# Kernel optimization log

Measured on AMD Instinct MI355X. Metric: run time of the kernel, lower is better.

Reference implementation:

```python
import jax, jax.numpy as jnp
import numpy as np


def conv2d(x, w, b):
    # x: [B, Cin, H, W], w: [Cout, Cin, 3, 3] -> SAME 3x3 conv, stride 1
    y = jax.lax.conv_general_dilated(x, w, (1, 1), 'SAME',
                                     dimension_numbers=('NCHW', 'OIHW', 'NCHW'))
    return y + b[None, :, None, None]


def trilinear_interpolation(data, offsets, sample_nums):
    """data: [B, D(frames), C, H, W]; offsets: [B, sample_nums*3, H, W]
    Returns samples [B, sample_nums, C, H, W] via trilinear interp over (d,h,w)."""
    B, D, C, H, W = data.shape
    S = sample_nums
    off = offsets.reshape(B, S, 3, H, W)
    # base 3x3x3 grid centered at middle frame / current pixel
    g = jnp.arange(S)
    kd = (g // 9 - 1).astype(jnp.float32)        # [S]
    kh = ((g // 3) % 3 - 1).astype(jnp.float32)
    kw = (g % 3 - 1).astype(jnp.float32)
    center = (D - 1) / 2.0
    hh = jnp.arange(H, dtype=jnp.float32)
    ww = jnp.arange(W, dtype=jnp.float32)
    pd = center + kd[None, :, None, None] + off[:, :, 0]                 # [B,S,H,W]
    ph = hh[None, None, :, None] + kh[None, :, None, None] + off[:, :, 1]
    pw = ww[None, None, None, :] + kw[None, :, None, None] + off[:, :, 2]
    pd = jnp.clip(pd, 0.0, D - 1.0)
    ph = jnp.clip(ph, 0.0, H - 1.0)
    pw = jnp.clip(pw, 0.0, W - 1.0)
    d0 = jnp.floor(pd); h0 = jnp.floor(ph); w0 = jnp.floor(pw)
    fd = pd - d0; fh = ph - h0; fw = pw - w0
    d0i = d0.astype(jnp.int32); h0i = h0.astype(jnp.int32); w0i = w0.astype(jnp.int32)
    d1i = jnp.minimum(d0i + 1, D - 1)
    h1i = jnp.minimum(h0i + 1, H - 1)
    w1i = jnp.minimum(w0i + 1, W - 1)
    # flatten (d,h,w) for gather, keep channels contiguous
    data_flat = data.transpose(0, 2, 1, 3, 4).reshape(B, C, D * H * W)

    def gather(di, hi, wi):
        idx = ((di * H + hi) * W + wi).reshape(B, 1, S * H * W)
        g_ = jnp.take_along_axis(data_flat, idx, axis=2)   # [B,C,S*H*W]
        return g_.reshape(B, C, S, H, W).transpose(0, 2, 1, 3, 4)  # [B,S,C,H,W]

    out = jnp.zeros((B, S, C, H, W), dtype=data.dtype)
    for di, wd in ((d0i, 1.0 - fd), (d1i, fd)):
        for hi, wh in ((h0i, 1.0 - fh), (h1i, fh)):
            for wi, wwgt in ((w0i, 1.0 - fw), (w1i, fw)):
                wgt = (wd * wh * wwgt)[:, :, None]  # [B,S,1,H,W]
                out = out + wgt * gather(di, hi, wi)
    return out


SAMPLE_NUMS = 27
GROUPS = 3


def setup_inputs() -> dict:
    key = jax.random.key(0)
    ks = jax.random.split(key, 14)
    B, BURST, C, H, W = 4, 5, 3, 256, 256
    in_len = BURST * C          # 15
    ch_w = in_len + 128 + SAMPLE_NUMS * C  # 224
    s = 0.05
    p = lambda k, sh: jax.random.normal(k, sh, dtype=jnp.float32) * s
    return {
        'data': jax.random.normal(ks[0], (B, BURST, C, H, W), dtype=jnp.float32),
        'enc_w1': p(ks[1], (64, in_len, 3, 3)), 'enc_b1': jnp.zeros((64,), jnp.float32),
        'enc_w2': p(ks[2], (128, 64, 3, 3)),    'enc_b2': jnp.zeros((128,), jnp.float32),
        'off_w':  p(ks[3], (SAMPLE_NUMS * 3, 128, 3, 3)), 'off_b': jnp.zeros((SAMPLE_NUMS * 3,), jnp.float32),
        'wc_w1':  p(ks[4], (64, ch_w, 3, 3)),   'wc_b1': jnp.zeros((64,), jnp.float32),
        'wc_w2':  p(ks[5], (64, 64, 3, 3)),     'wc_b2': jnp.zeros((64,), jnp.float32),
        'wc_w3':  p(ks[6], (SAMPLE_NUMS, 64, 3, 3)), 'wc_b3': jnp.zeros((SAMPLE_NUMS,), jnp.float32),
    }


def reference(data, enc_w1, enc_b1, enc_w2, enc_b2, off_w, off_b,
              wc_w1, wc_b1, wc_w2, wc_b2, wc_w3, wc_b3):
    B, D, C, H, W = data.shape
    net_feed = data.reshape(B, D * C, H, W)
    # encoder_decoder proxy: feature [B,128,H,W] + offsets [B,81,H,W]
    f1 = jax.nn.relu(conv2d(net_feed, enc_w1, enc_b1))
    feature = jax.nn.relu(conv2d(f1, enc_w2, enc_b2))
    offsets = conv2d(feature, off_w, off_b)
    samples = trilinear_interpolation(data, offsets, SAMPLE_NUMS)  # [B,S,C,H,W]
    weight_feed = jnp.concatenate([net_feed, feature,
                                   samples.reshape(B, SAMPLE_NUMS * C, H, W)], axis=1)
    h1 = jax.nn.relu(conv2d(weight_feed, wc_w1, wc_b1))
    h2 = jax.nn.relu(conv2d(h1, wc_w2, wc_b2))
    weights = conv2d(h2, wc_w3, wc_b3)  # [B,S,H,W]
    cpg = SAMPLE_NUMS // GROUPS
    s_g = samples.reshape(B, GROUPS, cpg, C, H, W)
    w_g = weights.reshape(B, GROUPS, cpg, H, W)
    # per-group weighted kernel-prediction sum (convolution_3D), scaled by g
    res_i = GROUPS * jnp.einsum('bgkchw,bgkhw->bgchw', s_g, w_g)
    out = jnp.sum(res_i, axis=1) / GROUPS
    return res_i, out, samples
```

## Files before the change

### kernel.cpp

```cpp
#include <hip/hip_runtime.h>


typedef __attribute__((ext_vector_type(8))) short short8;
typedef __attribute__((ext_vector_type(4))) float f32x4;

__device__ __forceinline__ unsigned short f2bf(float f) {
    unsigned int b = __float_as_uint(f);
    b = (b + 0x7fffu + ((b >> 16) & 1u)) >> 16;
    return (unsigned short)b;
}
__device__ __forceinline__ float bf2f(unsigned int u) {
    return __uint_as_float(u << 16);
}
__device__ __forceinline__ unsigned int pack2(float a, float b) {
    return (unsigned int)f2bf(a) | ((unsigned int)f2bf(b) << 16);
}

__global__ __launch_bounds__(256) void pack_w(
    const float* __restrict__ w, unsigned short* __restrict__ wp,
    int Cin_real, int Cout_real, int Cout_pad, int nch, int remap, int total)
{
    int idx = blockIdx.x * 256 + threadIdx.x;
    if (idx >= total) return;
    int kin = idx & 31;
    int t = idx >> 5;
    int co = t % Cout_pad; t /= Cout_pad;
    int chunk = t % nch;
    int tap = t / nch;
    int ci = chunk * 32 + kin;
    int cs = -1;
    if (remap) {
        if (ci < 15) cs = ci;
        else if (ci >= 16 && ci <= 224) cs = ci - 1;
    } else {
        if (ci < Cin_real) cs = ci;
    }
    float val = 0.f;
    if (co < Cout_real && cs >= 0)
        val = w[(co * Cin_real + cs) * 9 + tap];
    wp[idx] = f2bf(val);
}

__global__ __launch_bounds__(256) void convert_data(
    const float* __restrict__ data, unsigned short* __restrict__ concat)
{
    int i = blockIdx.x * 256 + threadIdx.x;
    int b = i >> 16, p = i & 65535;
    int base = i * 232;
#pragma unroll
    for (int c = 0; c < 15; ++c)
        concat[base + c] = f2bf(data[(b * 15 + c) * 65536 + p]);
    concat[base + 15] = 0;
}

__global__ __launch_bounds__(256) void conv_mfma(
    const unsigned short* __restrict__ src, int srcCs, int srcOff,
    const unsigned short* __restrict__ wp, const float* __restrict__ bias,
    int nch, int Cout, int Cout_pad,
    void* __restrict__ dst, int dstCs, int dstOff, int mode, int relu)
{
    __shared__ uint4 ldsb[816];
    const int tid = threadIdx.x;
    const int lane = tid & 63;
    const int wv = tid >> 6;
    const int wm = wv & 1, wn = wv >> 1;
    const int bx = blockIdx.x, b = blockIdx.y, bz = blockIdx.z;
    const int x0 = (bx & 7) * 32, y0 = (bx >> 3) * 4;
    const int l15 = lane & 15, l4 = lane >> 4;

    f32x4 acc[2][4];
#pragma unroll
    for (int mt = 0; mt < 2; ++mt)
#pragma unroll
        for (int nt = 0; nt < 4; ++nt) acc[mt][nt] = (f32x4)0.f;

    for (int chunk = 0; chunk < nch; ++chunk) {
        __syncthreads();
        for (int s = tid; s < 816; s += 256) {
            int kb = s / 204, hp = s - kb * 204;
            int hy = hp / 34, hx = hp - hy * 34;
            int y = y0 - 1 + hy, x = x0 - 1 + hx;
            int ch = srcOff + chunk * 32 + kb * 8;
            uint4 v = make_uint4(0u, 0u, 0u, 0u);
            if ((unsigned)y < 256u && (unsigned)x < 256u && ch + 8 <= srcCs)
                v = *(const uint4*)(src + ((b * 65536 + y * 256 + x) * srcCs + ch));
            ldsb[s] = v;
        }
        __syncthreads();
#pragma unroll
        for (int tap = 0; tap < 9; ++tap) {
            const int dy = tap / 3, dx = tap - dy * 3;
            short8 af[2];
#pragma unroll
            for (int mt = 0; mt < 2; ++mt) {
                int co = bz * 64 + wm * 32 + mt * 16 + l15;
                af[mt] = *(const short8*)(wp +
                    (((tap * nch + chunk) * Cout_pad + co) * 4 + l4) * 8);
            }
#pragma unroll
            for (int nt = 0; nt < 4; ++nt) {
                int p = wn * 64 + nt * 16;
                int hp = ((p >> 5) + dy) * 34 + (p & 31) + l15 + dx;
                short8 bf = __builtin_bit_cast(short8, ldsb[l4 * 204 + hp]);
#pragma unroll
                for (int mt = 0; mt < 2; ++mt)
                    acc[mt][nt] = __builtin_amdgcn_mfma_f32_16x16x32_bf16(
                        af[mt], bf, acc[mt][nt], 0, 0, 0);
            }
        }
    }

#pragma unroll
    for (int mt = 0; mt < 2; ++mt) {
        int co0 = bz * 64 + wm * 32 + mt * 16 + l4 * 4;
#pragma unroll
        for (int nt = 0; nt < 4; ++nt) {
            int p = wn * 64 + nt * 16 + l15;
            int y = y0 + (p >> 5), x = x0 + (p & 31);
            float v[4];
#pragma unroll
            for (int e = 0; e < 4; ++e) {
                int co = co0 + e;
                float f = acc[mt][nt][e] + ((co < Cout) ? bias[co] : 0.f);
                if (relu) f = fmaxf(f, 0.f);
                v[e] = f;
            }
            if (mode == 0) {
                unsigned short* d = (unsigned short*)dst +
                    ((b * 65536 + y * 256 + x) * dstCs + dstOff + co0);
                if (co0 + 3 < Cout) {
                    uint2 pk = make_uint2(pack2(v[0], v[1]), pack2(v[2], v[3]));
                    *(uint2*)d = pk;
                } else {
#pragma unroll
                    for (int e = 0; e < 4; ++e)
                        if (co0 + e < Cout) d[e] = f2bf(v[e]);
                }
            } else {
                float* d = (float*)dst + (b * dstCs + co0) * 65536 + y * 256 + x;
#pragma unroll
                for (int e = 0; e < 4; ++e)
                    if (co0 + e < Cout) d[e * 65536] = v[e];
            }
        }
    }
}

__global__ __launch_bounds__(256) void trilin_kern(
    const float* __restrict__ data, unsigned short* __restrict__ concat,
    float* __restrict__ smp)
{
    int i = blockIdx.x * 256 + threadIdx.x;
    int b = i >> 16, p = i & 65535;
    int y = p >> 8, x = p & 255;
    unsigned short* cptr = concat + i * 232 + 144;

    unsigned int wbuf[41];
    {
        const uint4* gp = (const uint4*)cptr;
#pragma unroll
        for (int k = 0; k < 10; ++k) {
            uint4 t = gp[k];
            wbuf[4 * k] = t.x; wbuf[4 * k + 1] = t.y;
            wbuf[4 * k + 2] = t.z; wbuf[4 * k + 3] = t.w;
        }
        wbuf[40] = (unsigned int)cptr[80];
    }

#pragma unroll
    for (int s = 0; s < 27; ++s) {
        int L0 = 3 * s;
        float o0 = bf2f((wbuf[L0 >> 1] >> ((L0 & 1) * 16)) & 0xffffu);
        float o1 = bf2f((wbuf[(L0 + 1) >> 1] >> (((L0 + 1) & 1) * 16)) & 0xffffu);
        float o2 = bf2f((wbuf[(L0 + 2) >> 1] >> (((L0 + 2) & 1) * 16)) & 0xffffu);

        float kd = (float)(s / 9 - 1);
        float kh = (float)((s / 3) % 3 - 1);
        float kw = (float)(s % 3 - 1);
        float pd = 2.0f + kd + o0;
        float ph = (float)y + kh + o1;
        float pw = (float)x + kw + o2;
        pd = fminf(fmaxf(pd, 0.f), 4.f);
        ph = fminf(fmaxf(ph, 0.f), 255.f);
        pw = fminf(fmaxf(pw, 0.f), 255.f);
        float d0 = floorf(pd), h0 = floorf(ph), w0 = floorf(pw);
        float fd = pd - d0, fh = ph - h0, fw = pw - w0;
        int d0i = (int)d0, h0i = (int)h0, w0i = (int)w0;
        int d1i = min(d0i + 1, 4), h1i = min(h0i + 1, 255), w1i = min(w0i + 1, 255);

        float res[3];
#pragma unroll
        for (int c = 0; c < 3; ++c) {
            const float* dp = data + ((b * 5 + d0i) * 3 + c) * 65536;
            const float* dp1 = data + ((b * 5 + d1i) * 3 + c) * 65536;
            int a00 = (h0i << 8) + w0i, a01 = (h0i << 8) + w1i;
            int a10 = (h1i << 8) + w0i, a11 = (h1i << 8) + w1i;
            float r0 = (dp[a00] * (1.f - fw) + dp[a01] * fw) * (1.f - fh)
                     + (dp[a10] * (1.f - fw) + dp[a11] * fw) * fh;
            float r1 = (dp1[a00] * (1.f - fw) + dp1[a01] * fw) * (1.f - fh)
                     + (dp1[a10] * (1.f - fw) + dp1[a11] * fw) * fh;
            float r = r0 * (1.f - fd) + r1 * fd;
            res[c] = r;
            smp[((b * 27 + s) * 3 + c) * 65536 + p] = r;
        }
#pragma unroll
        for (int c = 0; c < 3; ++c) {
            int L = L0 + c;
            unsigned int u = (unsigned int)f2bf(res[c]);
            if (L & 1) wbuf[L >> 1] = (wbuf[L >> 1] & 0xffffu) | (u << 16);
            else       wbuf[L >> 1] = (wbuf[L >> 1] & 0xffff0000u) | u;
        }
    }

    wbuf[40] &= 0xffffu;
    uint4* gp = (uint4*)cptr;
#pragma unroll
    for (int k = 0; k < 10; ++k)
        gp[k] = make_uint4(wbuf[4 * k], wbuf[4 * k + 1], wbuf[4 * k + 2], wbuf[4 * k + 3]);
    *(unsigned int*)(cptr + 80) = wbuf[40];
}

__global__ __launch_bounds__(256) void combine_kern(
    const float* __restrict__ smp, const float* __restrict__ wt,
    float* __restrict__ res_i, float* __restrict__ outp)
{
    int i = blockIdx.x * 256 + threadIdx.x;
    int p = i & 65535;
    int b = i >> 16;
    float ov[3] = {0.f, 0.f, 0.f};
#pragma unroll
    for (int g = 0; g < 3; ++g) {
        float r[3] = {0.f, 0.f, 0.f};
#pragma unroll
        for (int k = 0; k < 9; ++k) {
            int s = g * 9 + k;
            float w = wt[((b * 27 + s) << 16) + p];
#pragma unroll
            for (int c = 0; c < 3; ++c)
                r[c] = fmaf(smp[(((b * 27 + s) * 3 + c) << 16) + p], w, r[c]);
        }
#pragma unroll
        for (int c = 0; c < 3; ++c) {
            res_i[(((b * 3 + g) * 3 + c) << 16) + p] = 3.f * r[c];
            ov[c] += r[c];
        }
    }
#pragma unroll
    for (int c = 0; c < 3; ++c)
        outp[((b * 3 + c) << 16) + p] = ov[c];
}

extern "C" void kernel_launch(void* const* d_in, const int* in_sizes, int n_in,
                              void* d_out, int out_size, void* d_ws, size_t ws_size,
                              hipStream_t stream)
{
    const float* data   = (const float*)d_in[0];
    const float* enc_w1 = (const float*)d_in[1];
    const float* enc_b1 = (const float*)d_in[2];
    const float* enc_w2 = (const float*)d_in[3];
    const float* enc_b2 = (const float*)d_in[4];
    const float* off_w  = (const float*)d_in[5];
    const float* off_b  = (const float*)d_in[6];
    const float* wc_w1  = (const float*)d_in[7];
    const float* wc_b1  = (const float*)d_in[8];
    const float* wc_w2  = (const float*)d_in[9];
    const float* wc_b2  = (const float*)d_in[10];
    const float* wc_w3  = (const float*)d_in[11];
    const float* wc_b3  = (const float*)d_in[12];

    float* dout  = (float*)d_out;
    float* res_i = dout;
    float* outp  = dout + 2359296;
    float* smp   = dout + 3145728;

    char* ws = (char*)d_ws;
    unsigned short* concat = (unsigned short*)ws;
    unsigned short* buf_a  = (unsigned short*)(ws + 121634816);
    unsigned short* buf_b  = (unsigned short*)(ws + 155189248);
    unsigned short* wpk    = (unsigned short*)(ws + 188743680);
    unsigned short* wp1 = wpk;
    unsigned short* wp2 = wpk + 18432;
    unsigned short* wp3 = wpk + 92160;
    unsigned short* wp5 = wpk + 239616;
    unsigned short* wp6 = wpk + 387072;
    unsigned short* wp7 = wpk + 423936;
    float* wconv = (float*)buf_a;

    dim3 blk(256);

    pack_w<<<72, blk, 0, stream>>>(enc_w1, wp1, 15, 64, 64, 1, 0, 18432);
    pack_w<<<288, blk, 0, stream>>>(enc_w2, wp2, 64, 128, 128, 2, 0, 73728);
    pack_w<<<576, blk, 0, stream>>>(off_w, wp3, 128, 81, 128, 4, 0, 147456);
    pack_w<<<576, blk, 0, stream>>>(wc_w1, wp5, 224, 64, 64, 8, 1, 147456);
    pack_w<<<144, blk, 0, stream>>>(wc_w2, wp6, 64, 64, 64, 2, 0, 36864);
    pack_w<<<144, blk, 0, stream>>>(wc_w3, wp7, 64, 27, 64, 2, 0, 36864);
    convert_data<<<1024, blk, 0, stream>>>(data, concat);

    conv_mfma<<<dim3(512, 4, 1), blk, 0, stream>>>(
        concat, 232, 0, wp1, enc_b1, 1, 64, 64, buf_a, 64, 0, 0, 1);
    conv_mfma<<<dim3(512, 4, 2), blk, 0, stream>>>(
        buf_a, 64, 0, wp2, enc_b2, 2, 128, 128, concat, 232, 16, 0, 1);
    conv_mfma<<<dim3(512, 4, 2), blk, 0, stream>>>(
        concat, 232, 16, wp3, off_b, 4, 81, 128, concat, 232, 144, 0, 0);
    trilin_kern<<<1024, blk, 0, stream>>>(data, concat, smp);
    conv_mfma<<<dim3(512, 4, 1), blk, 0, stream>>>(
        concat, 232, 0, wp5, wc_b1, 8, 64, 64, buf_a, 64, 0, 0, 1);
    conv_mfma<<<dim3(512, 4, 1), blk, 0, stream>>>(
        buf_a, 64, 0, wp6, wc_b2, 2, 64, 64, buf_b, 64, 0, 0, 1);
    conv_mfma<<<dim3(512, 4, 1), blk, 0, stream>>>(
        buf_b, 64, 0, wp7, wc_b3, 2, 27, 64, wconv, 27, 0, 1, 0);
    combine_kern<<<1024, blk, 0, stream>>>(smp, wconv, res_i, outp);
}
```

Measured before the change: 819.6 us.

## Double-buffer conv tiles with direct global-to-LDS loads and larger pixel tiles

The MFMA conv kernel now stages input halos with global_load_lds straight into a double-buffered LDS tile, prefetching the next channel chunk while the current one is computed. Each block covers 64x4 pixels, and each wave owns one row and all 64 output channels, which doubles weight-fragment reuse. Out-of-range halo loads read from a zero pad in the workspace. M tiles beyond the real Cout are skipped, so padded output channels get no MFMA work. The six weight-packing launches are merged into one kernel. The risks are higher register and LDS use, which lowers occupancy, and only half as many blocks per conv.

```diff
diff --git a/kernel.cpp b/kernel.cpp
--- a/kernel.cpp
+++ b/kernel.cpp
@@ -16,29 +16,42 @@
     return (unsigned int)f2bf(a) | ((unsigned int)f2bf(b) << 16);
 }
 
-__global__ __launch_bounds__(256) void pack_w(
-    const float* __restrict__ w, unsigned short* __restrict__ wp,
-    int Cin_real, int Cout_real, int Cout_pad, int nch, int remap, int total)
+__global__ __launch_bounds__(256) void prep_kern(
+    const float* __restrict__ w1, const float* __restrict__ w2,
+    const float* __restrict__ w3, const float* __restrict__ w5,
+    const float* __restrict__ w6, const float* __restrict__ w7,
+    unsigned short* __restrict__ wpk)
 {
     int idx = blockIdx.x * 256 + threadIdx.x;
-    if (idx >= total) return;
-    int kin = idx & 31;
-    int t = idx >> 5;
-    int co = t % Cout_pad; t /= Cout_pad;
-    int chunk = t % nch;
-    int tap = t / nch;
-    int ci = chunk * 32 + kin;
-    int cs = -1;
-    if (remap) {
-        if (ci < 15) cs = ci;
-        else if (ci >= 16 && ci <= 224) cs = ci - 1;
-    } else {
-        if (ci < Cin_real) cs = ci;
-    }
-    float val = 0.f;
-    if (co < Cout_real && cs >= 0)
-        val = w[(co * Cin_real + cs) * 9 + tap];
-    wp[idx] = f2bf(val);
+    if (idx < 460800) {
+        const float* w; int off, CinR, CoutR, CoutP, nch, remap;
+        if (idx < 18432)       { w = w1; off = 0;      CinR = 15;  CoutR = 64;  CoutP = 64;  nch = 1; remap = 0; }
+        else if (idx < 92160)  { w = w2; off = 18432;  CinR = 64;  CoutR = 128; CoutP = 128; nch = 2; remap = 0; }
+        else if (idx < 239616) { w = w3; off = 92160;  CinR = 128; CoutR = 81;  CoutP = 128; nch = 4; remap = 0; }
+        else if (idx < 387072) { w = w5; off = 239616; CinR = 224; CoutR = 64;  CoutP = 64;  nch = 8; remap = 1; }
+        else if (idx < 423936) { w = w6; off = 387072; CinR = 64;  CoutR = 64;  CoutP = 64;  nch = 2; remap = 0; }
+        else                   { w = w7; off = 423936; CinR = 64;  CoutR = 27;  CoutP = 64;  nch = 2; remap = 0; }
+        int li = idx - off;
+        int kin = li & 31;
+        int t = li >> 5;
+        int co = t % CoutP; t /= CoutP;
+        int chunk = t % nch;
+        int tap = t / nch;
+        int ci = chunk * 32 + kin;
+        int cs = -1;
+        if (remap) {
+            if (ci < 15) cs = ci;
+            else if (ci >= 16 && ci <= 224) cs = ci - 1;
+        } else {
+            if (ci < CinR) cs = ci;
+        }
+        float val = 0.f;
+        if (co < CoutR && cs >= 0)
+            val = w[(co * CinR + cs) * 9 + tap];
+        wpk[idx] = f2bf(val);
+    } else if (idx < 460800 + 8192) {
+        wpk[idx] = 0;
+    }
 }
 
 __global__ __launch_bounds__(256) void convert_data(
@@ -57,71 +70,90 @@
     const unsigned short* __restrict__ src, int srcCs, int srcOff,
     const unsigned short* __restrict__ wp, const float* __restrict__ bias,
     int nch, int Cout, int Cout_pad,
-    void* __restrict__ dst, int dstCs, int dstOff, int mode, int relu)
-{
-    __shared__ uint4 ldsb[816];
+    void* __restrict__ dst, int dstCs, int dstOff, int mode, int relu,
+    const uint4* __restrict__ zp)
+{
+    __shared__ uint4 ldsb[2][1584];
     const int tid = threadIdx.x;
     const int lane = tid & 63;
     const int wv = tid >> 6;
-    const int wm = wv & 1, wn = wv >> 1;
     const int bx = blockIdx.x, b = blockIdx.y, bz = blockIdx.z;
-    const int x0 = (bx & 7) * 32, y0 = (bx >> 3) * 4;
+    const int x0 = (bx & 3) * 64, y0 = (bx >> 2) * 4;
     const int l15 = lane & 15, l4 = lane >> 4;
-
-    f32x4 acc[2][4];
-#pragma unroll
-    for (int mt = 0; mt < 2; ++mt)
-#pragma unroll
-        for (int nt = 0; nt < 4; ++nt) acc[mt][nt] = (f32x4)0.f;
-
-    for (int chunk = 0; chunk < nch; ++chunk) {
+    const int mtc = min(4, (Cout - bz * 64 + 15) >> 4);
+
+    f32x4 acc[4][4];
+#pragma unroll
+    for (int m = 0; m < 4; ++m)
+#pragma unroll
+        for (int nt = 0; nt < 4; ++nt) acc[m][nt] = (f32x4)0.f;
+
+    auto stage = [&](int buf, int chunk) {
+        int ch = srcOff + chunk * 32 + wv * 8;
+        bool chok = (ch + 8 <= srcCs);
+        const unsigned short* sbase = src + ch;
+#pragma unroll
+        for (int it = 0; it < 7; ++it) {
+            int r = it * 64 + lane;
+            if (r < 396) {
+                int hy = r / 66, hx = r - hy * 66;
+                int y = y0 - 1 + hy, x = x0 - 1 + hx;
+                const uint4* g;
+                if (chok && (unsigned)y < 256u && (unsigned)x < 256u)
+                    g = (const uint4*)(sbase + (b * 65536 + y * 256 + x) * srcCs);
+                else
+                    g = zp + lane;
+                __builtin_amdgcn_global_load_lds(
+                    (const __attribute__((address_space(1))) void*)g,
+                    (__attribute__((address_space(3))) void*)&ldsb[buf][wv * 396 + it * 64],
+                    16, 0, 0);
+            }
+        }
+    };
+
+    stage(0, 0);
+    int buf = 0;
+    for (int c = 0; c < nch; ++c) {
         __syncthreads();
-        for (int s = tid; s < 816; s += 256) {
-            int kb = s / 204, hp = s - kb * 204;
-            int hy = hp / 34, hx = hp - hy * 34;
-            int y = y0 - 1 + hy, x = x0 - 1 + hx;
-            int ch = srcOff + chunk * 32 + kb * 8;
-            uint4 v = make_uint4(0u, 0u, 0u, 0u);
-            if ((unsigned)y < 256u && (unsigned)x < 256u && ch + 8 <= srcCs)
-                v = *(const uint4*)(src + ((b * 65536 + y * 256 + x) * srcCs + ch));
-            ldsb[s] = v;
-        }
-        __syncthreads();
+        if (c + 1 < nch) stage(buf ^ 1, c + 1);
 #pragma unroll
         for (int tap = 0; tap < 9; ++tap) {
             const int dy = tap / 3, dx = tap - dy * 3;
-            short8 af[2];
-#pragma unroll
-            for (int mt = 0; mt < 2; ++mt) {
-                int co = bz * 64 + wm * 32 + mt * 16 + l15;
-                af[mt] = *(const short8*)(wp +
-                    (((tap * nch + chunk) * Cout_pad + co) * 4 + l4) * 8);
+            short8 af[4];
+#pragma unroll
+            for (int m = 0; m < 4; ++m)
+                if (m < mtc)
+                    af[m] = *(const short8*)(wp +
+                        ((tap * nch + c) * Cout_pad + bz * 64 + m * 16 + l15) * 32 + l4 * 8);
+#pragma unroll
+            for (int nt = 0; nt < 4; ++nt) {
+                int hx = nt * 16 + l15 + dx;
+                int hy = wv + dy;
+                short8 bf = __builtin_bit_cast(short8,
+                    ldsb[buf][l4 * 396 + hy * 66 + hx]);
+#pragma unroll
+                for (int m = 0; m < 4; ++m)
+                    if (m < mtc)
+                        acc[m][nt] = __builtin_amdgcn_mfma_f32_16x16x32_bf16(
+                            af[m], bf, acc[m][nt], 0, 0, 0);
             }
-#pragma unroll
-            for (int nt = 0; nt < 4; ++nt) {
-                int p = wn * 64 + nt * 16;
-                int hp = ((p >> 5) + dy) * 34 + (p & 31) + l15 + dx;
-                short8 bf = __builtin_bit_cast(short8, ldsb[l4 * 204 + hp]);
-#pragma unroll
-                for (int mt = 0; mt < 2; ++mt)
-                    acc[mt][nt] = __builtin_amdgcn_mfma_f32_16x16x32_bf16(
-                        af[mt], bf, acc[mt][nt], 0, 0, 0);
-            }
-        }
-    }
-
-#pragma unroll
-    for (int mt = 0; mt < 2; ++mt) {
-        int co0 = bz * 64 + wm * 32 + mt * 16 + l4 * 4;
+        }
+        buf ^= 1;
+    }
+
+    const int y = y0 + wv;
+#pragma unroll
+    for (int m = 0; m < 4; ++m) {
+        if (m >= mtc) continue;
+        int co0 = bz * 64 + m * 16 + l4 * 4;
 #pragma unroll
         for (int nt = 0; nt < 4; ++nt) {
-            int p = wn * 64 + nt * 16 + l15;
-            int y = y0 + (p >> 5), x = x0 + (p & 31);
+            int x = x0 + nt * 16 + l15;
             float v[4];
 #pragma unroll
             for (int e = 0; e < 4; ++e) {
                 int co = co0 + e;
-                float f = acc[mt][nt][e] + ((co < Cout) ? bias[co] : 0.f);
+                float f = acc[m][nt][e] + ((co < Cout) ? bias[co] : 0.f);
                 if (relu) f = fmaxf(f, 0.f);
                 v[e] = f;
             }
@@ -284,30 +316,26 @@
     unsigned short* wp5 = wpk + 239616;
     unsigned short* wp6 = wpk + 387072;
     unsigned short* wp7 = wpk + 423936;
+    const uint4* zp = (const uint4*)(wpk + 460800);
     float* wconv = (float*)buf_a;
 
     dim3 blk(256);
 
-    pack_w<<<72, blk, 0, stream>>>(enc_w1, wp1, 15, 64, 64, 1, 0, 18432);
-    pack_w<<<288, blk, 0, stream>>>(enc_w2, wp2, 64, 128, 128, 2, 0, 73728);
-    pack_w<<<576, blk, 0, stream>>>(off_w, wp3, 128, 81, 128, 4, 0, 147456);
-    pack_w<<<576, blk, 0, stream>>>(wc_w1, wp5, 224, 64, 64, 8, 1, 147456);
-    pack_w<<<144, blk, 0, stream>>>(wc_w2, wp6, 64, 64, 64, 2, 0, 36864);
-    pack_w<<<144, blk, 0, stream>>>(wc_w3, wp7, 64, 27, 64, 2, 0, 36864);
+    prep_kern<<<1832, blk, 0, stream>>>(enc_w1, enc_w2, off_w, wc_w1, wc_w2, wc_w3, wpk);
     convert_data<<<1024, blk, 0, stream>>>(data, concat);
 
-    conv_mfma<<<dim3(512, 4, 1), blk, 0, stream>>>(
-        concat, 232, 0, wp1, enc_b1, 1, 64, 64, buf_a, 64, 0, 0, 1);
-    conv_mfma<<<dim3(512, 4, 2), blk, 0, stream>>>(
-        buf_a, 64, 0, wp2, enc_b2, 2, 128, 128, concat, 232, 16, 0, 1);
-    conv_mfma<<<dim3(512, 4, 2), blk, 0, stream>>>(
-        concat, 232, 16, wp3, off_b, 4, 81, 128, concat, 232, 144, 0, 0);
+    conv_mfma<<<dim3(256, 4, 1), blk, 0, stream>>>(
+        concat, 232, 0, wp1, enc_b1, 1, 64, 64, buf_a, 64, 0, 0, 1, zp);
+    conv_mfma<<<dim3(256, 4, 2), blk, 0, stream>>>(
+        buf_a, 64, 0, wp2, enc_b2, 2, 128, 128, concat, 232, 16, 0, 1, zp);
+    conv_mfma<<<dim3(256, 4, 2), blk, 0, stream>>>(
+        concat, 232, 16, wp3, off_b, 4, 81, 128, concat, 232, 144, 0, 0, zp);
     trilin_kern<<<1024, blk, 0, stream>>>(data, concat, smp);
-    conv_mfma<<<dim3(512, 4, 1), blk, 0, stream>>>(
-        concat, 232, 0, wp5, wc_b1, 8, 64, 64, buf_a, 64, 0, 0, 1);
-    conv_mfma<<<dim3(512, 4, 1), blk, 0, stream>>>(
-        buf_a, 64, 0, wp6, wc_b2, 2, 64, 64, buf_b, 64, 0, 0, 1);
-    conv_mfma<<<dim3(512, 4, 1), blk, 0, stream>>>(
-        buf_b, 64, 0, wp7, wc_b3, 2, 27, 64, wconv, 27, 0, 1, 0);
+    conv_mfma<<<dim3(256, 4, 1), blk, 0, stream>>>(
+        concat, 232, 0, wp5, wc_b1, 8, 64, 64, buf_a, 64, 0, 0, 1, zp);
+    conv_mfma<<<dim3(256, 4, 1), blk, 0, stream>>>(
+        buf_a, 64, 0, wp6, wc_b2, 2, 64, 64, buf_b, 64, 0, 0, 1, zp);
+    conv_mfma<<<dim3(256, 4, 1), blk, 0, stream>>>(
+        buf_b, 64, 0, wp7, wc_b3, 2, 27, 64, wconv, 27, 0, 1, 0, zp);
     combine_kern<<<1024, blk, 0, stream>>>(smp, wconv, res_i, outp);
 }
```

New measurement: 814.5 us. About the same (-0.6%).
